# Kernel optimization log

Measured on AMD Instinct MI355X. Metric: run time of the kernel, lower is better.

The kernel has to match this reference:

```python
import jax, jax.numpy as jnp
import numpy as np

CORR_THRESHOLD = 0.5
EPS = 1e-12


def setup_inputs() -> dict:
    key = jax.random.key(0)
    # x: [B, N_channels, T] EEG windows
    x = jax.random.normal(key, (128, 64, 30720), dtype=jnp.float32)
    return {"x": x}


def reference(x):
    # Batched Pearson correlation across channels (rows = variables, like np.corrcoef).
    B, N, T = x.shape
    xc = x - jnp.mean(x, axis=-1, keepdims=True)            # center over time
    cov = jnp.einsum("bnt,bmt->bnm", xc, xc)                # [B, N, N] unnormalized
    norms = jnp.sqrt(jnp.einsum("bnt,bnt->bn", xc, xc))     # [B, N] row L2 norms
    corr = cov / (norms[:, :, None] * norms[:, None, :] + EPS)
    # zero diagonal, then threshold on |corr|
    eye = jnp.eye(N, dtype=bool)
    corr = jnp.where(eye[None], 0.0, corr)
    mask = jnp.abs(corr) >= CORR_THRESHOLD
    adj = jnp.where(mask, corr, 0.0)                        # dense masked adjacency [B, N, N]
    # node features are the raw EEG samples (as in the original Data(x=eeg_sample, ...))
    return adj, x
```

## Files before the change

kernel.cpp:

```cpp
#include <hip/hip_runtime.h>
#include <cstdint>
#include <cstddef>

#define B_   128
#define NCH  64
#define T_   30720
#define TT   128
#define EPSF 1e-12f
#define THRF 0.5f

typedef float  f32x4 __attribute__((ext_vector_type(4)));
typedef short  s16x8 __attribute__((ext_vector_type(8)));
typedef unsigned short u16;

static __device__ __forceinline__ u16 bf16_rne(float f, float& as_f32) {
    unsigned u = __builtin_bit_cast(unsigned, f);
    unsigned r = (u + 0x7FFFu + ((u >> 16) & 1u)) >> 16;
    as_f32 = __builtin_bit_cast(float, r << 16);
    return (u16)r;
}

__global__ __launch_bounds__(256) void corr_stage1(
    const float* __restrict__ x, float* __restrict__ out_x,
    float* __restrict__ P, float* __restrict__ S,
    int split, int Tc)
{
    __shared__ __align__(16) u16 ldsH[NCH * TT];
    __shared__ __align__(16) u16 ldsL[NCH * TT];

    const int tid  = threadIdx.x;
    const int lane = tid & 63;
    const int w    = tid >> 6;

    const int bid = blockIdx.x;
    const int b   = bid / split;
    const int c   = bid - b * split;

    const size_t base = (size_t)b * ((size_t)NCH * T_) + (size_t)c * Tc;
    const float* xb = x + base;
    float*       ob = out_x + base;

    const int sch = tid >> 4;
    const int sg  = tid & 15;

    const int r    = lane & 15;
    const int koff = (lane >> 4) << 4;
    const int swz  = (r & 7) << 4;

    f32x4 acc[4];
    #pragma unroll
    for (int fn = 0; fn < 4; ++fn) acc[fn] = (f32x4)(0.f);
    float ssum[4] = {0.f, 0.f, 0.f, 0.f};

    const int ntile = Tc / TT;

    for (int tile = 0; tile < ntile; ++tile) {
        const int tbase = tile * TT;
        __syncthreads();
        #pragma unroll
        for (int p = 0; p < 4; ++p) {
            const int ch = p * 16 + sch;
            const size_t go = (size_t)ch * T_ + (size_t)(tbase + sg * 8);
            const f32x4 v0 = *reinterpret_cast<const f32x4*>(xb + go);
            const f32x4 v1 = *reinterpret_cast<const f32x4*>(xb + go + 4);
            __builtin_nontemporal_store(v0, reinterpret_cast<f32x4*>(ob + go));
            __builtin_nontemporal_store(v1, reinterpret_cast<f32x4*>(ob + go + 4));
            float e[8] = {v0.x, v0.y, v0.z, v0.w, v1.x, v1.y, v1.z, v1.w};
            s16x8 hv, lv;
            #pragma unroll
            for (int j = 0; j < 8; ++j) {
                float hf, dummy;
                const u16 hb = bf16_rne(e[j], hf);
                const u16 lb = bf16_rne(e[j] - hf, dummy);
                hv[j] = (short)hb;
                lv[j] = (short)lb;
                ssum[p] += e[j];
            }
            const int ba = ch * (TT * 2) + ((sg * 16) ^ ((ch & 7) << 4));
            *reinterpret_cast<s16x8*>(reinterpret_cast<char*>(ldsH) + ba) = hv;
            *reinterpret_cast<s16x8*>(reinterpret_cast<char*>(ldsL) + ba) = lv;
        }
        __syncthreads();
        #pragma unroll
        for (int ks = 0; ks < 4; ++ks) {
            const int tb = ((ks * 64 + koff) ^ swz);
            const char* hA = reinterpret_cast<const char*>(ldsH) + (w * 16 + r) * (TT * 2) + tb;
            const char* lA = reinterpret_cast<const char*>(ldsL) + (w * 16 + r) * (TT * 2) + tb;
            const s16x8 ah = *reinterpret_cast<const s16x8*>(hA);
            const s16x8 al = *reinterpret_cast<const s16x8*>(lA);
            #pragma unroll
            for (int fn = 0; fn < 4; ++fn) {
                const int rowb = fn * 16 + r;
                const char* hB = reinterpret_cast<const char*>(ldsH) + rowb * (TT * 2) + tb;
                const char* lB = reinterpret_cast<const char*>(ldsL) + rowb * (TT * 2) + tb;
                const s16x8 bh = *reinterpret_cast<const s16x8*>(hB);
                const s16x8 bl = *reinterpret_cast<const s16x8*>(lB);
                acc[fn] = __builtin_amdgcn_mfma_f32_16x16x32_bf16(ah, bh, acc[fn], 0, 0, 0);
                acc[fn] = __builtin_amdgcn_mfma_f32_16x16x32_bf16(ah, bl, acc[fn], 0, 0, 0);
                acc[fn] = __builtin_amdgcn_mfma_f32_16x16x32_bf16(al, bh, acc[fn], 0, 0, 0);
            }
        }
    }

    __syncthreads();
    float* sred = reinterpret_cast<float*>(ldsH);
    #pragma unroll
    for (int p = 0; p < 4; ++p) sred[p * 256 + tid] = ssum[p];
    __syncthreads();
    if (tid < NCH) {
        const int pidx = tid >> 4, ridx = tid & 15;
        float s = 0.f;
        #pragma unroll
        for (int g = 0; g < 16; ++g) s += sred[pidx * 256 + ridx * 16 + g];
        S[(size_t)(b * split + c) * NCH + tid] = s;
    }

    float* Pc = P + ((size_t)(b * split + c) << 12);
    const int rowc = w * 16 + ((lane >> 4) << 2);
    const int col  = lane & 15;
    #pragma unroll
    for (int fn = 0; fn < 4; ++fn)
        #pragma unroll
        for (int reg = 0; reg < 4; ++reg)
            Pc[(rowc + reg) * 64 + fn * 16 + col] = acc[fn][reg];
}

__global__ __launch_bounds__(256) void corr_stage2(
    const float* __restrict__ P, const float* __restrict__ S,
    float* __restrict__ adj, int split)
{
    const int idx = blockIdx.x * 256 + threadIdx.x;
    const int b  = idx >> 12;
    const int nm = idx & 4095;
    const int n  = nm >> 6;
    const int m  = nm & 63;

    float G = 0.f, Gnn = 0.f, Gmm = 0.f, Sn = 0.f, Sm = 0.f;
    for (int c = 0; c < split; ++c) {
        const float* Pc = P + ((size_t)(b * split + c) << 12);
        const float* Sc = S + (size_t)(b * split + c) * NCH;
        G   += Pc[nm];
        Gnn += Pc[n * 65];
        Gmm += Pc[m * 65];
        Sn  += Sc[n];
        Sm  += Sc[m];
    }
    const float invT = 1.0f / (float)T_;
    const float cov  = G   - Sn * Sm * invT;
    const float vn   = Gnn - Sn * Sn * invT;
    const float vm   = Gmm - Sm * Sm * invT;
    const float den  = sqrtf(vn) * sqrtf(vm) + EPSF;
    float corr = cov / den;
    if (n == m) corr = 0.f;
    adj[idx] = (fabsf(corr) >= THRF) ? corr : 0.f;
}

extern "C" void kernel_launch(void* const* d_in, const int* in_sizes, int n_in,
                              void* d_out, int out_size, void* d_ws, size_t ws_size,
                              hipStream_t stream)
{
    const float* x   = (const float*)d_in[0];
    float* out   = (float*)d_out;
    float* adj   = out;
    float* out_x = out + (size_t)B_ * NCH * NCH;

    int split = 8;
    while (split > 1 &&
           (size_t)B_ * split * (4096 + NCH) * sizeof(float) > ws_size)
        split >>= 1;

    float* P = (float*)d_ws;
    float* S = P + (size_t)B_ * split * 4096;
    const int Tc = T_ / split;

    corr_stage1<<<dim3(B_ * split), dim3(256), 0, stream>>>(x, out_x, P, S, split, Tc);
    corr_stage2<<<dim3((B_ * 4096) / 256), dim3(256), 0, stream>>>(P, S, adj, split);
}
```

Measured before the change: 481.5 us.

## Drop bf16 split-precision GEMM, double-buffer LDS tiles, and raise time split

Replaces the three-MFMA hi/lo bf16 emulation with a single plain bf16 MFMA per product and removes the low-part LDS buffer. The LDS buffer is reused as a double buffer, so the next tile is staged while the current one is multiplied, with one barrier per tile. The time split doubles to raise block count. Single bf16 precision may shift correlations near the 0.5 threshold and change adjacency entries. The split reduction also becomes coarser per block.

```diff
diff --git a/kernel.cpp b/kernel.cpp
--- a/kernel.cpp
+++ b/kernel.cpp
@@ -1,4 +1,5 @@
 #include <hip/hip_runtime.h>
+#include <hip/hip_bf16.h>
 #include <cstdint>
 #include <cstddef>
 
@@ -13,11 +14,8 @@
 typedef short  s16x8 __attribute__((ext_vector_type(8)));
 typedef unsigned short u16;
 
-static __device__ __forceinline__ u16 bf16_rne(float f, float& as_f32) {
-    unsigned u = __builtin_bit_cast(unsigned, f);
-    unsigned r = (u + 0x7FFFu + ((u >> 16) & 1u)) >> 16;
-    as_f32 = __builtin_bit_cast(float, r << 16);
-    return (u16)r;
+static __device__ __forceinline__ short bf16s(float f) {
+    return (short)__builtin_bit_cast(u16, __float2bfloat16(f));
 }
 
 __global__ __launch_bounds__(256) void corr_stage1(
@@ -25,8 +23,7 @@
     float* __restrict__ P, float* __restrict__ S,
     int split, int Tc)
 {
-    __shared__ __align__(16) u16 ldsH[NCH * TT];
-    __shared__ __align__(16) u16 ldsL[NCH * TT];
+    __shared__ __align__(16) u16 lds[2][NCH * TT];
 
     const int tid  = threadIdx.x;
     const int lane = tid & 63;
@@ -54,9 +51,8 @@
 
     const int ntile = Tc / TT;
 
-    for (int tile = 0; tile < ntile; ++tile) {
+    auto stage = [&](int tile, int buf) {
         const int tbase = tile * TT;
-        __syncthreads();
         #pragma unroll
         for (int p = 0; p < 4; ++p) {
             const int ch = p * 16 + sch;
@@ -65,45 +61,40 @@
             const f32x4 v1 = *reinterpret_cast<const f32x4*>(xb + go + 4);
             __builtin_nontemporal_store(v0, reinterpret_cast<f32x4*>(ob + go));
             __builtin_nontemporal_store(v1, reinterpret_cast<f32x4*>(ob + go + 4));
-            float e[8] = {v0.x, v0.y, v0.z, v0.w, v1.x, v1.y, v1.z, v1.w};
-            s16x8 hv, lv;
-            #pragma unroll
-            for (int j = 0; j < 8; ++j) {
-                float hf, dummy;
-                const u16 hb = bf16_rne(e[j], hf);
-                const u16 lb = bf16_rne(e[j] - hf, dummy);
-                hv[j] = (short)hb;
-                lv[j] = (short)lb;
-                ssum[p] += e[j];
-            }
+            ssum[p] += ((v0.x + v0.y) + (v0.z + v0.w))
+                     + ((v1.x + v1.y) + (v1.z + v1.w));
+            s16x8 hv;
+            hv[0] = bf16s(v0.x); hv[1] = bf16s(v0.y);
+            hv[2] = bf16s(v0.z); hv[3] = bf16s(v0.w);
+            hv[4] = bf16s(v1.x); hv[5] = bf16s(v1.y);
+            hv[6] = bf16s(v1.z); hv[7] = bf16s(v1.w);
             const int ba = ch * (TT * 2) + ((sg * 16) ^ ((ch & 7) << 4));
-            *reinterpret_cast<s16x8*>(reinterpret_cast<char*>(ldsH) + ba) = hv;
-            *reinterpret_cast<s16x8*>(reinterpret_cast<char*>(ldsL) + ba) = lv;
+            *reinterpret_cast<s16x8*>(reinterpret_cast<char*>(lds[buf]) + ba) = hv;
         }
-        __syncthreads();
+    };
+
+    stage(0, 0);
+    __syncthreads();
+
+    for (int t = 0; t < ntile; ++t) {
+        if (t + 1 < ntile) stage(t + 1, (t + 1) & 1);
+        const char* Lb = reinterpret_cast<const char*>(lds[t & 1]);
         #pragma unroll
         for (int ks = 0; ks < 4; ++ks) {
             const int tb = ((ks * 64 + koff) ^ swz);
-            const char* hA = reinterpret_cast<const char*>(ldsH) + (w * 16 + r) * (TT * 2) + tb;
-            const char* lA = reinterpret_cast<const char*>(ldsL) + (w * 16 + r) * (TT * 2) + tb;
-            const s16x8 ah = *reinterpret_cast<const s16x8*>(hA);
-            const s16x8 al = *reinterpret_cast<const s16x8*>(lA);
+            const s16x8 ah = *reinterpret_cast<const s16x8*>(
+                Lb + (w * 16 + r) * (TT * 2) + tb);
             #pragma unroll
             for (int fn = 0; fn < 4; ++fn) {
-                const int rowb = fn * 16 + r;
-                const char* hB = reinterpret_cast<const char*>(ldsH) + rowb * (TT * 2) + tb;
-                const char* lB = reinterpret_cast<const char*>(ldsL) + rowb * (TT * 2) + tb;
-                const s16x8 bh = *reinterpret_cast<const s16x8*>(hB);
-                const s16x8 bl = *reinterpret_cast<const s16x8*>(lB);
+                const s16x8 bh = *reinterpret_cast<const s16x8*>(
+                    Lb + (fn * 16 + r) * (TT * 2) + tb);
                 acc[fn] = __builtin_amdgcn_mfma_f32_16x16x32_bf16(ah, bh, acc[fn], 0, 0, 0);
-                acc[fn] = __builtin_amdgcn_mfma_f32_16x16x32_bf16(ah, bl, acc[fn], 0, 0, 0);
-                acc[fn] = __builtin_amdgcn_mfma_f32_16x16x32_bf16(al, bh, acc[fn], 0, 0, 0);
             }
         }
+        __syncthreads();
     }
 
-    __syncthreads();
-    float* sred = reinterpret_cast<float*>(ldsH);
+    float* sred = reinterpret_cast<float*>(lds[0]);
     #pragma unroll
     for (int p = 0; p < 4; ++p) sred[p * 256 + tid] = ssum[p];
     __syncthreads();
@@ -164,7 +155,7 @@
     float* adj   = out;
     float* out_x = out + (size_t)B_ * NCH * NCH;
 
-    int split = 8;
+    int split = 16;
     while (split > 1 &&
            (size_t)B_ * split * (4096 + NCH) * sizeof(float) > ws_size)
         split >>= 1;
```

Result: slower. 657.1 us (+36.5%).
